# Kernel tuning notes

Hardware: AMD Instinct MI355X
Metric: run time of the kernel (lower is better)

The kernel has to match this reference:

```python
import jax, jax.numpy as jnp
import numpy as np

EPS = 1e-12  # torch F.normalize eps
SIGMA_RBF = 1.0  # rbf bandwidth (init arg sigma=1)


def _l2norm(v, axis=-1):
    return v / jnp.maximum(jnp.linalg.norm(v, axis=axis, keepdims=True), EPS)


def setup_inputs() -> dict:
    key = jax.random.key(0)
    kx, kw, kb, ku, kc = jax.random.split(key, 5)
    B, C, E, F = 512, 100, 2048, 128
    x = jax.random.normal(kx, (B, E), dtype=jnp.float32)
    # per-class Linear weights [C, F, E] and biases [C, F] (torch Linear layout: out x in)
    bound = 1.0 / np.sqrt(E)
    W = jax.random.uniform(kw, (C, F, E), minval=-bound, maxval=bound, dtype=jnp.float32)
    b = jax.random.uniform(kb, (C, F), minval=-bound, maxval=bound, dtype=jnp.float32)
    # spectral-norm power-iteration vectors u (one per class, normalized)
    u = _l2norm(jax.random.normal(ku, (C, F), dtype=jnp.float32))
    # centroid buffer c (EMA means; randn stand-in for a trained state)
    c = jax.random.normal(kc, (C, F), dtype=jnp.float32)
    return {"x": x, "W": W, "b": b, "u": u, "c": c}


def reference(x, W, b, u, c):
    # --- spectral norm: one power-iteration step per class (torch default) ---
    v = _l2norm(jnp.einsum('cfe,cf->ce', W, u))        # v = normalize(W^T u)  [C,E]
    u2 = _l2norm(jnp.einsum('cfe,ce->cf', W, v))       # u = normalize(W v)    [C,F]
    sigma = jnp.einsum('cf,cfe,ce->c', u2, W, v)       # sigma = u^T W v       [C]
    Wn = W / sigma[:, None, None]
    # --- fused per-class linear projections: z[b,c,f] ---
    z = jnp.einsum('be,cfe->bcf', x, Wn) + b[None, :, :]
    # --- RBF to centroids: exp(-||c - z||^2 / (2 sigma^2)) ---
    dist2 = jnp.sum((c[None, :, :] - z) ** 2, axis=-1)  # [B, C]
    probs = jnp.exp(-dist2 / (2.0 * SIGMA_RBF ** 2))
    return probs
```

## Files before the change

### kernel.cpp

```cpp
#include <hip/hip_runtime.h>
#include <math.h>

#define B_ 512
#define C_ 100
#define E_ 2048
#define F_ 128
#define NCHUNK 16
#define CHUNKW 128

typedef _Float16 f16x8 __attribute__((ext_vector_type(8)));
typedef float    f32x4 __attribute__((ext_vector_type(4)));

#define AS1q __attribute__((address_space(1)))
#define AS3q __attribute__((address_space(3)))

__device__ __forceinline__ void gl_lds16(const void* g, void* lds_base) {
    __builtin_amdgcn_global_load_lds((const AS1q void*)g, (AS3q void*)lds_base, 16, 0, 0);
}

__device__ __forceinline__ f16x8 frag_ld(const float* T, int r, int p) {
    const int k = r & 15;
    const int b = r << 6;
    const f32x4 lo = *(const f32x4*)&T[b + ((((p << 1))     ^ k) << 2)];
    const f32x4 hi = *(const f32x4*)&T[b + ((((p << 1) | 1) ^ k) << 2)];
    f16x8 fr;
    fr[0] = (_Float16)lo[0]; fr[1] = (_Float16)lo[1];
    fr[2] = (_Float16)lo[2]; fr[3] = (_Float16)lo[3];
    fr[4] = (_Float16)hi[0]; fr[5] = (_Float16)hi[1];
    fr[6] = (_Float16)hi[2]; fr[7] = (_Float16)hi[3];
    return fr;
}

__global__ __launch_bounds__(256, 3)
void k_gram(const float* __restrict__ W, _Float16* __restrict__ Wh,
            const float* __restrict__ x, _Float16* __restrict__ xh,
            const float* __restrict__ u, float* __restrict__ ychunks) {
    const int b = blockIdx.x;
    const int t = threadIdx.x;

    if (b >= 1600) {
        const size_t base = (size_t)(b - 1600) * 32768 + t * 8;
#pragma unroll
        for (int it = 0; it < 16; ++it) {
            const size_t idx = base + (size_t)it * 2048;
            float4 a  = *(const float4*)(x + idx);
            float4 bb = *(const float4*)(x + idx + 4);
            f16x8 h;
            h[0] = (_Float16)a.x;  h[1] = (_Float16)a.y;  h[2] = (_Float16)a.z;  h[3] = (_Float16)a.w;
            h[4] = (_Float16)bb.x; h[5] = (_Float16)bb.y; h[6] = (_Float16)bb.z; h[7] = (_Float16)bb.w;
            *(f16x8*)(xh + idx) = h;
        }
        return;
    }

    const int c     = b >> 4;
    const int chunk = b & 15;
    const int w  = t >> 6;
    const int l  = t & 63;
    const int wm = w & 1, wn = w >> 1;
    const int ln = l & 15, quad = l >> 4;

    __shared__ float Ts[128 * 64];

    f32x4 acc[4][4];
#pragma unroll
    for (int mt = 0; mt < 4; ++mt)
#pragma unroll
        for (int nt = 0; nt < 4; ++nt) acc[mt][nt] = (f32x4){0.f, 0.f, 0.f, 0.f};

    const int lrow4 = l >> 4, cs = l & 15;
    const float* wbase = W + (size_t)c * F_ * E_ + chunk * CHUNKW;

    const int cr = t >> 1, cb = (t & 1) * 32;
    _Float16* wdst = Wh + ((size_t)c * F_ + cr) * E_ + chunk * CHUNKW + cb;

#pragma unroll
    for (int it = 0; it < CHUNKW / 64; ++it) {
        const int k0 = it * 64;
#pragma unroll
        for (int qq = 0; qq < 8; ++qq) {
            const int q   = w * 8 + qq;
            const int r   = q * 4 + lrow4;
            const int off = ((cs ^ (r & 15)) << 2);
            gl_lds16(wbase + (size_t)r * E_ + k0 + off, &Ts[q * 256]);
        }
        __syncthreads();

        {
            f32x4 v[8];
#pragma unroll
            for (int j = 0; j < 8; ++j) {
                const int g = (cb >> 2) + j;
                v[j] = *(const f32x4*)&Ts[cr * 64 + ((g ^ (cr & 15)) << 2)];
            }
#pragma unroll
            for (int j = 0; j < 4; ++j) {
                f16x8 h;
                h[0] = (_Float16)v[2*j][0]; h[1] = (_Float16)v[2*j][1];
                h[2] = (_Float16)v[2*j][2]; h[3] = (_Float16)v[2*j][3];
                h[4] = (_Float16)v[2*j+1][0]; h[5] = (_Float16)v[2*j+1][1];
                h[6] = (_Float16)v[2*j+1][2]; h[7] = (_Float16)v[2*j+1][3];
                *(f16x8*)(wdst + k0 + j * 8) = h;
            }
        }

#pragma unroll
        for (int kk = 0; kk < 64; kk += 32) {
            const int pb = quad + (kk >> 3);
            f16x8 av[4], bv[4];
#pragma unroll
            for (int mt = 0; mt < 4; ++mt)
                av[mt] = frag_ld(Ts, wm * 64 + mt * 16 + ln, pb);
#pragma unroll
            for (int nt = 0; nt < 4; ++nt)
                bv[nt] = frag_ld(Ts, wn * 64 + nt * 16 + ln, pb);
#pragma unroll
            for (int mt = 0; mt < 4; ++mt)
#pragma unroll
                for (int nt = 0; nt < 4; ++nt)
                    acc[mt][nt] = __builtin_amdgcn_mfma_f32_16x16x32_f16(
                        av[mt], bv[nt], acc[mt][nt], 0, 0, 0);
        }
        __syncthreads();
    }

    const float* uc = u + (size_t)c * F_;
    float un[4];
#pragma unroll
    for (int nt = 0; nt < 4; ++nt) un[nt] = uc[wn * 64 + nt * 16 + ln];

    float* red = (float*)&Ts[0];

#pragma unroll
    for (int mt = 0; mt < 4; ++mt) {
#pragma unroll
        for (int rr = 0; rr < 4; ++rr) {
            float py = acc[mt][0][rr] * un[0];
            py = fmaf(acc[mt][1][rr], un[1], py);
            py = fmaf(acc[mt][2][rr], un[2], py);
            py = fmaf(acc[mt][3][rr], un[3], py);
            py += __shfl_xor(py, 1, 64);
            py += __shfl_xor(py, 2, 64);
            py += __shfl_xor(py, 4, 64);
            py += __shfl_xor(py, 8, 64);
            if (ln == 0) {
                int m = wm * 64 + mt * 16 + quad * 4 + rr;
                red[m * 2 + wn] = py;
            }
        }
    }
    __syncthreads();
    if (t < 128) {
        float yv = red[t * 2] + red[t * 2 + 1];
        ychunks[((size_t)chunk * C_ + c) * F_ + t] = yv;
    }
}

__global__ __launch_bounds__(256, 3)
void k_main(const _Float16* __restrict__ xh, const _Float16* __restrict__ Wh,
            const float* __restrict__ bias, const float* __restrict__ cent,
            const float* __restrict__ u, const float* __restrict__ ychunks,
            float* __restrict__ out) {
    const int c  = blockIdx.y;
    const int b0 = blockIdx.x * 128;
    const int t  = threadIdx.x;
    const int w  = t >> 6;
    const int l  = t & 63;
    const int wm = w & 1, wn = w >> 1;
    const int ln = l & 15, quad = l >> 4;

    __shared__ _Float16 Xs[128 * 64];
    __shared__ _Float16 Ws[128 * 64];
    __shared__ float red2[2][2];
    __shared__ float s_rsig;

    if (t < 128) {
        float yf = 0.f;
#pragma unroll
        for (int ch = 0; ch < NCHUNK; ++ch)
            yf += ychunks[((size_t)ch * C_ + c) * F_ + t];
        float nvp = u[(size_t)c * F_ + t] * yf;
        float tsp = yf * yf;
        for (int off = 32; off; off >>= 1) {
            nvp += __shfl_down(nvp, off, 64);
            tsp += __shfl_down(tsp, off, 64);
        }
        if (l == 0) { red2[w][0] = nvp; red2[w][1] = tsp; }
    }
    __syncthreads();
    if (t == 0) s_rsig = sqrtf((red2[0][0] + red2[1][0]) / (red2[0][1] + red2[1][1]));

    f32x4 acc[4][4];
#pragma unroll
    for (int mt = 0; mt < 4; ++mt)
#pragma unroll
        for (int nt = 0; nt < 4; ++nt) acc[mt][nt] = (f32x4){0.f, 0.f, 0.f, 0.f};

    const int lr = l >> 3;
    const int lg = (l & 7) ^ lr;
    const _Float16* xsrc = xh + (size_t)(b0 + w * 32 + lr) * E_ + lg * 8;
    const _Float16* wsrc = Wh + ((size_t)c * F_ + w * 32 + lr) * E_ + lg * 8;

    for (int k0 = 0; k0 < E_; k0 += 64) {
#pragma unroll
        for (int q = 0; q < 4; ++q)
            gl_lds16(xsrc + (size_t)q * 8 * E_ + k0, &Xs[(w * 4 + q) * 512]);
#pragma unroll
        for (int q = 0; q < 4; ++q)
            gl_lds16(wsrc + (size_t)q * 8 * E_ + k0, &Ws[(w * 4 + q) * 512]);
        __syncthreads();

#pragma unroll
        for (int kk = 0; kk < 64; kk += 32) {
            const int g0 = (kk >> 3) + quad;
            const int sw = (g0 ^ (ln & 7)) * 8;
            f16x8 av[4], bv[4];
#pragma unroll
            for (int mt = 0; mt < 4; ++mt)
                av[mt] = *(const f16x8*)&Xs[(wm * 64 + mt * 16 + ln) * 64 + sw];
#pragma unroll
            for (int nt = 0; nt < 4; ++nt)
                bv[nt] = *(const f16x8*)&Ws[(wn * 64 + nt * 16 + ln) * 64 + sw];
#pragma unroll
            for (int mt = 0; mt < 4; ++mt)
#pragma unroll
                for (int nt = 0; nt < 4; ++nt)
                    acc[mt][nt] = __builtin_amdgcn_mfma_f32_16x16x32_f16(
                        av[mt], bv[nt], acc[mt][nt], 0, 0, 0);
        }
        __syncthreads();
    }

    const float rsigma = s_rsig;

    float bi[4], ce[4];
#pragma unroll
    for (int nt = 0; nt < 4; ++nt) {
        int f = wn * 64 + nt * 16 + ln;
        bi[nt] = bias[c * F_ + f];
        ce[nt] = cent[c * F_ + f];
    }

    float* red = (float*)&Xs[0];

#pragma unroll
    for (int mt = 0; mt < 4; ++mt) {
#pragma unroll
        for (int r = 0; r < 4; ++r) {
            float part = 0.f;
#pragma unroll
            for (int nt = 0; nt < 4; ++nt) {
                float z = fmaf(acc[mt][nt][r], rsigma, bi[nt]);
                float d = ce[nt] - z;
                part = fmaf(d, d, part);
            }
            part += __shfl_xor(part, 1, 64);
            part += __shfl_xor(part, 2, 64);
            part += __shfl_xor(part, 4, 64);
            part += __shfl_xor(part, 8, 64);
            if (ln == 0) {
                int m = wm * 64 + mt * 16 + quad * 4 + r;
                red[m * 2 + wn] = part;
            }
        }
    }
    __syncthreads();
    if (t < 128) {
        float d2 = red[t * 2] + red[t * 2 + 1];
        out[(size_t)(b0 + t) * C_ + c] = expf(-0.5f * d2);
    }
}

extern "C" void kernel_launch(void* const* d_in, const int* in_sizes, int n_in,
                              void* d_out, int out_size, void* d_ws, size_t ws_size,
                              hipStream_t stream) {
    const float* x  = (const float*)d_in[0];
    const float* W  = (const float*)d_in[1];
    const float* b  = (const float*)d_in[2];
    const float* u  = (const float*)d_in[3];
    const float* cc = (const float*)d_in[4];
    float* out = (float*)d_out;

    char* ws = (char*)d_ws;
    _Float16* Wh      = (_Float16*)ws;
    _Float16* xh      = (_Float16*)(ws + (size_t)C_ * F_ * E_ * 2);
    float*    ychunks = (float*)(ws + (size_t)C_ * F_ * E_ * 2 + (size_t)B_ * E_ * 2);

    k_gram<<<1632, 256, 0, stream>>>(W, Wh, x, xh, u, ychunks);

    dim3 grid(B_ / 128, C_);
    k_main<<<grid, 256, 0, stream>>>(xh, Wh, b, cc, u, ychunks, out);
}
```

Before: 216.6 us.

## Retile main GEMM to 64x128 blocks with two waves owning full F rows

The main kernel now uses 128-thread blocks, each covering 64 batch rows by all 128 features. Each wave computes 32 rows across the full F dimension, so the squared-distance reduction finishes inside the wave and writes the output directly, with no cross-wave LDS reduction or extra barrier. The grid doubles to 800 blocks, which improves occupancy and load balance on the CUs. In exchange, W tiles are reloaded twice as often from global memory, and each wave holds 16 accumulators and 8 B fragments per k-step.

```diff
diff --git a/kernel.cpp b/kernel.cpp
--- a/kernel.cpp
+++ b/kernel.cpp
@@ -156,25 +156,24 @@
     }
 }
 
-__global__ __launch_bounds__(256, 3)
+__global__ __launch_bounds__(128, 3)
 void k_main(const _Float16* __restrict__ xh, const _Float16* __restrict__ Wh,
             const float* __restrict__ bias, const float* __restrict__ cent,
             const float* __restrict__ u, const float* __restrict__ ychunks,
             float* __restrict__ out) {
     const int c  = blockIdx.y;
-    const int b0 = blockIdx.x * 128;
+    const int b0 = blockIdx.x * 64;
     const int t  = threadIdx.x;
     const int w  = t >> 6;
     const int l  = t & 63;
-    const int wm = w & 1, wn = w >> 1;
     const int ln = l & 15, quad = l >> 4;
 
-    __shared__ _Float16 Xs[128 * 64];
+    __shared__ _Float16 Xs[64 * 64];
     __shared__ _Float16 Ws[128 * 64];
     __shared__ float red2[2][2];
     __shared__ float s_rsig;
 
-    if (t < 128) {
+    {
         float yf = 0.f;
 #pragma unroll
         for (int ch = 0; ch < NCHUNK; ++ch)
@@ -190,41 +189,45 @@
     __syncthreads();
     if (t == 0) s_rsig = sqrtf((red2[0][0] + red2[1][0]) / (red2[0][1] + red2[1][1]));
 
-    f32x4 acc[4][4];
-#pragma unroll
-    for (int mt = 0; mt < 4; ++mt)
-#pragma unroll
-        for (int nt = 0; nt < 4; ++nt) acc[mt][nt] = (f32x4){0.f, 0.f, 0.f, 0.f};
+    f32x4 acc[2][8];
+#pragma unroll
+    for (int mt = 0; mt < 2; ++mt)
+#pragma unroll
+        for (int nt = 0; nt < 8; ++nt) acc[mt][nt] = (f32x4){0.f, 0.f, 0.f, 0.f};
 
     const int lr = l >> 3;
     const int lg = (l & 7) ^ lr;
-    const _Float16* xsrc = xh + (size_t)(b0 + w * 32 + lr) * E_ + lg * 8;
-    const _Float16* wsrc = Wh + ((size_t)c * F_ + w * 32 + lr) * E_ + lg * 8;
+    const _Float16* xsrc = xh + (size_t)b0 * E_ + (size_t)lr * E_ + lg * 8;
+    const _Float16* wsrc = Wh + (size_t)c * F_ * E_ + (size_t)lr * E_ + lg * 8;
 
     for (int k0 = 0; k0 < E_; k0 += 64) {
 #pragma unroll
-        for (int q = 0; q < 4; ++q)
-            gl_lds16(xsrc + (size_t)q * 8 * E_ + k0, &Xs[(w * 4 + q) * 512]);
-#pragma unroll
-        for (int q = 0; q < 4; ++q)
-            gl_lds16(wsrc + (size_t)q * 8 * E_ + k0, &Ws[(w * 4 + q) * 512]);
+        for (int qq = 0; qq < 4; ++qq) {
+            const int q = w * 4 + qq;
+            gl_lds16(xsrc + (size_t)q * 8 * E_ + k0, &Xs[q * 512]);
+        }
+#pragma unroll
+        for (int qq = 0; qq < 8; ++qq) {
+            const int q = w * 8 + qq;
+            gl_lds16(wsrc + (size_t)q * 8 * E_ + k0, &Ws[q * 512]);
+        }
         __syncthreads();
 
 #pragma unroll
         for (int kk = 0; kk < 64; kk += 32) {
             const int g0 = (kk >> 3) + quad;
             const int sw = (g0 ^ (ln & 7)) * 8;
-            f16x8 av[4], bv[4];
-#pragma unroll
-            for (int mt = 0; mt < 4; ++mt)
-                av[mt] = *(const f16x8*)&Xs[(wm * 64 + mt * 16 + ln) * 64 + sw];
-#pragma unroll
-            for (int nt = 0; nt < 4; ++nt)
-                bv[nt] = *(const f16x8*)&Ws[(wn * 64 + nt * 16 + ln) * 64 + sw];
-#pragma unroll
-            for (int mt = 0; mt < 4; ++mt)
-#pragma unroll
-                for (int nt = 0; nt < 4; ++nt)
+            f16x8 av[2], bv[8];
+#pragma unroll
+            for (int mt = 0; mt < 2; ++mt)
+                av[mt] = *(const f16x8*)&Xs[(w * 32 + mt * 16 + ln) * 64 + sw];
+#pragma unroll
+            for (int nt = 0; nt < 8; ++nt)
+                bv[nt] = *(const f16x8*)&Ws[(nt * 16 + ln) * 64 + sw];
+#pragma unroll
+            for (int mt = 0; mt < 2; ++mt)
+#pragma unroll
+                for (int nt = 0; nt < 8; ++nt)
                     acc[mt][nt] = __builtin_amdgcn_mfma_f32_16x16x32_f16(
                         av[mt], bv[nt], acc[mt][nt], 0, 0, 0);
         }
@@ -233,23 +236,21 @@
 
     const float rsigma = s_rsig;
 
-    float bi[4], ce[4];
-#pragma unroll
-    for (int nt = 0; nt < 4; ++nt) {
-        int f = wn * 64 + nt * 16 + ln;
+    float bi[8], ce[8];
+#pragma unroll
+    for (int nt = 0; nt < 8; ++nt) {
+        int f = nt * 16 + ln;
         bi[nt] = bias[c * F_ + f];
         ce[nt] = cent[c * F_ + f];
     }
 
-    float* red = (float*)&Xs[0];
-
-#pragma unroll
-    for (int mt = 0; mt < 4; ++mt) {
+#pragma unroll
+    for (int mt = 0; mt < 2; ++mt) {
 #pragma unroll
         for (int r = 0; r < 4; ++r) {
             float part = 0.f;
 #pragma unroll
-            for (int nt = 0; nt < 4; ++nt) {
+            for (int nt = 0; nt < 8; ++nt) {
                 float z = fmaf(acc[mt][nt][r], rsigma, bi[nt]);
                 float d = ce[nt] - z;
                 part = fmaf(d, d, part);
@@ -259,15 +260,10 @@
             part += __shfl_xor(part, 4, 64);
             part += __shfl_xor(part, 8, 64);
             if (ln == 0) {
-                int m = wm * 64 + mt * 16 + quad * 4 + r;
-                red[m * 2 + wn] = part;
-            }
-        }
-    }
-    __syncthreads();
-    if (t < 128) {
-        float d2 = red[t * 2] + red[t * 2 + 1];
-        out[(size_t)(b0 + t) * C_ + c] = expf(-0.5f * d2);
+                int m = w * 32 + mt * 16 + quad * 4 + r;
+                out[(size_t)(b0 + m) * C_ + c] = expf(-0.5f * part);
+            }
+        }
     }
 }
 
@@ -288,6 +284,6 @@
 
     k_gram<<<1632, 256, 0, stream>>>(W, Wh, x, xh, u, ychunks);
 
-    dim3 grid(B_ / 128, C_);
-    k_main<<<grid, 256, 0, stream>>>(xh, Wh, b, cc, u, ychunks, out);
-}
+    dim3 grid(B_ / 64, C_);
+    k_main<<<grid, 128, 0, stream>>>(xh, Wh, b, cc, u, ychunks, out);
+}
```

Result: slower. 244.7 us (+13.0%).
